# Performance work log

Measured on AMD Instinct MI355X. Metric: run time of the kernel, lower is better.

Reference implementation:

```python
import jax, jax.numpy as jnp
import numpy as np

C = 192          # filter_channels (= in_channels in this module)
K = 3            # kernel_size
NB = 10          # num_bins of rational-quadratic spline (VITS default)
TB = 5.0         # tail_bound
NF = 4           # number of ConvFlow steps per branch
L = 3            # DDSConv n_layers
LOG2PI = float(np.log(2.0 * np.pi))


def conv1x1(x, w, b):
    # x: (B, Cin, T), w: (Cout, Cin)
    return jnp.einsum('oi,bit->bot', w, x) + b[None, :, None]


def depthwise(x, w, b, dil):
    # x: (B, C, T), w: (C, 1, K), dilated depthwise conv, 'same' padding
    pad = dil * (K - 1) // 2
    y = jax.lax.conv_general_dilated(
        x, w, window_strides=(1,), padding=[(pad, pad)], rhs_dilation=(dil,),
        dimension_numbers=('NCH', 'OIH', 'NCH'), feature_group_count=x.shape[1])
    return y + b[None, :, None]


def layer_norm_c(x, g, b, eps=1e-5):
    # VITS LayerNorm: normalize over the channel axis (axis=1)
    m = jnp.mean(x, axis=1, keepdims=True)
    v = jnp.mean((x - m) ** 2, axis=1, keepdims=True)
    return (x - m) * jax.lax.rsqrt(v + eps) * g[None, :, None] + b[None, :, None]


def dds(x, x_mask, g, dep_w, dep_b, pw_w, pw_b, ln_g, ln_b):
    # DDSConv: dilated depth-separable conv stack with residual
    if g is not None:
        x = x + g
    for i in range(L):
        dil = K ** i
        y = depthwise(x * x_mask, dep_w[i], dep_b[i], dil)
        y = jax.nn.gelu(layer_norm_c(y, ln_g[i, 0], ln_b[i, 0]))
        y = conv1x1(y, pw_w[i], pw_b[i])
        y = jax.nn.gelu(layer_norm_c(y, ln_g[i, 1], ln_b[i, 1]))
        x = x + y  # dropout disabled in deterministic reference
    return x * x_mask


def ew_affine(z, x_mask, m, logs):
    y = (m[None, :, None] + jnp.exp(logs)[None, :, None] * z) * x_mask
    ld = jnp.sum(logs[None, :, None] * x_mask, axis=(1, 2))
    return y, ld


def rqs_forward(x_in, uw, uh, ud):
    # unconstrained rational-quadratic spline, forward direction, linear tails
    mb = 1e-3  # min bin width / height / derivative
    const = float(np.log(np.expm1(1.0 - mb)))
    inside = (x_in >= -TB) & (x_in <= TB)
    ud = jnp.pad(ud, ((0, 0), (0, 0), (0, 0), (1, 1)), constant_values=const)
    wd = jax.nn.softmax(uw, -1); wd = mb + (1.0 - mb * NB) * wd
    cw = jnp.cumsum(wd, -1)
    cw = jnp.concatenate([jnp.zeros_like(cw[..., :1]), cw], -1)
    cw = 2.0 * TB * cw - TB
    cw = cw.at[..., 0].set(-TB).at[..., -1].set(TB)
    wd = cw[..., 1:] - cw[..., :-1]
    ht = jax.nn.softmax(uh, -1); ht = mb + (1.0 - mb * NB) * ht
    ch = jnp.cumsum(ht, -1)
    ch = jnp.concatenate([jnp.zeros_like(ch[..., :1]), ch], -1)
    ch = 2.0 * TB * ch - TB
    ch = ch.at[..., 0].set(-TB).at[..., -1].set(TB)
    ht = ch[..., 1:] - ch[..., :-1]
    dv = mb + jax.nn.softplus(ud)  # (..., NB+1)
    xc = jnp.clip(x_in, -TB, TB)
    idx = jnp.clip(jnp.sum((xc[..., None] >= cw[..., :-1]).astype(jnp.int32), -1) - 1, 0, NB - 1)
    g = lambda a, i: jnp.take_along_axis(a, i[..., None], -1)[..., 0]
    icw, iw, ich, ih = g(cw, idx), g(wd, idx), g(ch, idx), g(ht, idx)
    idelta = ih / iw
    d0, d1 = g(dv, idx), g(dv, idx + 1)
    th = (xc - icw) / iw
    t1m = th * (1.0 - th)
    den = idelta + (d0 + d1 - 2.0 * idelta) * t1m
    out = ich + ih * (idelta * th * th + d0 * t1m) / den
    dnum = idelta * idelta * (d1 * th * th + 2.0 * idelta * t1m + d0 * (1.0 - th) ** 2)
    lad = jnp.log(dnum) - 2.0 * jnp.log(den)
    return jnp.where(inside, out, x_in), jnp.where(inside, lad, 0.0)


def conv_flow(z, x_mask, g, pre_w, pre_b, dep_w, dep_b, pw_w, pw_b, ln_g, ln_b, proj_w, proj_b):
    x0, x1 = z[:, :1], z[:, 1:]  # (B,1,T) each
    h = conv1x1(x0, pre_w, pre_b)
    h = dds(h, x_mask, g, dep_w, dep_b, pw_w, pw_b, ln_g, ln_b)
    h = conv1x1(h, proj_w, proj_b) * x_mask      # (B, 3*NB-1, T)
    B, _, T = h.shape
    h = h.reshape(B, 1, 3 * NB - 1, T).transpose(0, 1, 3, 2)  # (B,1,T,3*NB-1)
    s = 1.0 / np.sqrt(C)
    x1n, lad = rqs_forward(x1, h[..., :NB] * s, h[..., NB:2 * NB] * s, h[..., 2 * NB:])
    zo = jnp.concatenate([x0, x1n], 1) * x_mask
    return zo, jnp.sum(lad * x_mask, axis=(1, 2))


def _forward(x, x_mask, w, e_q, pre_w, pre_b, proj_w, proj_b,
             dds_dep_w, dds_dep_b, dds_pw_w, dds_pw_b, dds_ln_g, dds_ln_b,
             post_pre_w, post_pre_b, post_proj_w, post_proj_b,
             pdds_dep_w, pdds_dep_b, pdds_pw_w, pdds_pw_b, pdds_ln_g, pdds_ln_b,
             aff_m, aff_logs,
             f_pre_w, f_pre_b, f_dep_w, f_dep_b, f_pw_w, f_pw_b, f_ln_g, f_ln_b, f_proj_w, f_proj_b,
             paff_m, paff_logs,
             p_pre_w, p_pre_b, p_dep_w, p_dep_b, p_pw_w, p_pw_b, p_ln_g, p_ln_b, p_proj_w, p_proj_b):
    x = jax.lax.stop_gradient(x)
    h = conv1x1(x, pre_w, pre_b)
    h = dds(h, x_mask, None, dds_dep_w, dds_dep_b, dds_pw_w, dds_pw_b, dds_ln_g, dds_ln_b)
    h = conv1x1(h, proj_w, proj_b) * x_mask
    hw = conv1x1(w, post_pre_w, post_pre_b)
    hw = dds(hw, x_mask, None, pdds_dep_w, pdds_dep_b, pdds_pw_w, pdds_pw_b, pdds_ln_g, pdds_ln_b)
    hw = conv1x1(hw, post_proj_w, post_proj_b) * x_mask
    e = e_q * x_mask
    zq, ldq = ew_affine(e, x_mask, paff_m, paff_logs)
    gp = h + hw
    for i in range(NF):
        zq, ld = conv_flow(zq, x_mask, gp, p_pre_w[i], p_pre_b[i], p_dep_w[i], p_dep_b[i],
                           p_pw_w[i], p_pw_b[i], p_ln_g[i], p_ln_b[i], p_proj_w[i], p_proj_b[i])
        ldq = ldq + ld
        zq = zq[:, ::-1]  # Flip (logdet 0)
    zu, z1 = zq[:, :1], zq[:, 1:]
    u = jax.nn.sigmoid(zu) * x_mask
    z0 = (w - u) * x_mask
    ldq = ldq + jnp.sum((jax.nn.log_sigmoid(zu) + jax.nn.log_sigmoid(-zu)) * x_mask, axis=(1, 2))
    logq = jnp.sum(-0.5 * (LOG2PI + e * e) * x_mask, axis=(1, 2)) - ldq
    y0 = jnp.log(jnp.maximum(z0, 1e-5)) * x_mask  # Log flow
    ldt = jnp.sum(-y0, axis=(1, 2))
    z = jnp.concatenate([y0, z1], 1)
    z, ld = ew_affine(z, x_mask, aff_m, aff_logs)
    ldt = ldt + ld
    for i in range(NF):
        z, ld = conv_flow(z, x_mask, h, f_pre_w[i], f_pre_b[i], f_dep_w[i], f_dep_b[i],
                          f_pw_w[i], f_pw_b[i], f_ln_g[i], f_ln_b[i], f_proj_w[i], f_proj_b[i])
        ldt = ldt + ld
        z = z[:, ::-1]
    nll = jnp.sum(0.5 * (LOG2PI + z * z) * x_mask, axis=(1, 2)) - ldt
    return nll + logq  # (B,)


def setup_inputs() -> dict:
    key = jax.random.key(0)
    ks = jax.random.split(key, 24)
    B, T = 32, 768
    P = 3 * NB - 1
    r = lambda k, shape, s=0.05: jax.random.normal(k, shape, jnp.float32) * s
    d = {}
    d['x'] = jax.random.normal(ks[0], (B, C, T), jnp.float32)
    d['x_mask'] = jnp.ones((B, 1, T), jnp.float32)
    d['w'] = jax.random.uniform(ks[1], (B, 1, T), jnp.float32) * 10.0 + 1.0  # positive durations
    d['e_q'] = jax.random.normal(ks[2], (B, 2, T), jnp.float32)
    d['pre_w'] = r(ks[3], (C, C)); d['pre_b'] = jnp.zeros((C,), jnp.float32)
    d['proj_w'] = r(ks[4], (C, C)); d['proj_b'] = jnp.zeros((C,), jnp.float32)
    d['dds_dep_w'] = r(ks[5], (L, C, 1, K)); d['dds_dep_b'] = jnp.zeros((L, C), jnp.float32)
    d['dds_pw_w'] = r(ks[6], (L, C, C)); d['dds_pw_b'] = jnp.zeros((L, C), jnp.float32)
    d['dds_ln_g'] = jnp.ones((L, 2, C), jnp.float32); d['dds_ln_b'] = jnp.zeros((L, 2, C), jnp.float32)
    d['post_pre_w'] = r(ks[7], (C, 1)); d['post_pre_b'] = jnp.zeros((C,), jnp.float32)
    d['post_proj_w'] = r(ks[8], (C, C)); d['post_proj_b'] = jnp.zeros((C,), jnp.float32)
    d['pdds_dep_w'] = r(ks[9], (L, C, 1, K)); d['pdds_dep_b'] = jnp.zeros((L, C), jnp.float32)
    d['pdds_pw_w'] = r(ks[10], (L, C, C)); d['pdds_pw_b'] = jnp.zeros((L, C), jnp.float32)
    d['pdds_ln_g'] = jnp.ones((L, 2, C), jnp.float32); d['pdds_ln_b'] = jnp.zeros((L, 2, C), jnp.float32)
    d['aff_m'] = r(ks[11], (2,)); d['aff_logs'] = r(ks[12], (2,))
    d['f_pre_w'] = r(ks[13], (NF, C, 1)); d['f_pre_b'] = jnp.zeros((NF, C), jnp.float32)
    d['f_dep_w'] = r(ks[14], (NF, L, C, 1, K)); d['f_dep_b'] = jnp.zeros((NF, L, C), jnp.float32)
    d['f_pw_w'] = r(ks[15], (NF, L, C, C)); d['f_pw_b'] = jnp.zeros((NF, L, C), jnp.float32)
    d['f_ln_g'] = jnp.ones((NF, L, 2, C), jnp.float32); d['f_ln_b'] = jnp.zeros((NF, L, 2, C), jnp.float32)
    d['f_proj_w'] = r(ks[16], (NF, P, C), 0.01); d['f_proj_b'] = jnp.zeros((NF, P), jnp.float32)
    d['paff_m'] = r(ks[17], (2,)); d['paff_logs'] = r(ks[18], (2,))
    d['p_pre_w'] = r(ks[19], (NF, C, 1)); d['p_pre_b'] = jnp.zeros((NF, C), jnp.float32)
    d['p_dep_w'] = r(ks[20], (NF, L, C, 1, K)); d['p_dep_b'] = jnp.zeros((NF, L, C), jnp.float32)
    d['p_pw_w'] = r(ks[21], (NF, L, C, C)); d['p_pw_b'] = jnp.zeros((NF, L, C), jnp.float32)
    d['p_ln_g'] = jnp.ones((NF, L, 2, C), jnp.float32); d['p_ln_b'] = jnp.zeros((NF, L, 2, C), jnp.float32)
    d['p_proj_w'] = r(ks[22], (NF, P, C), 0.01); d['p_proj_b'] = jnp.zeros((NF, P), jnp.float32)
    return d


def reference(x, x_mask, w, e_q, pre_w, pre_b, proj_w, proj_b,
              dds_dep_w, dds_dep_b, dds_pw_w, dds_pw_b, dds_ln_g, dds_ln_b,
              post_pre_w, post_pre_b, post_proj_w, post_proj_b,
              pdds_dep_w, pdds_dep_b, pdds_pw_w, pdds_pw_b, pdds_ln_g, pdds_ln_b,
              aff_m, aff_logs,
              f_pre_w, f_pre_b, f_dep_w, f_dep_b, f_pw_w, f_pw_b, f_ln_g, f_ln_b, f_proj_w, f_proj_b,
              paff_m, paff_logs,
              p_pre_w, p_pre_b, p_dep_w, p_dep_b, p_pw_w, p_pw_b, p_ln_g, p_ln_b, p_proj_w, p_proj_b):
    return _forward(x, x_mask, w, e_q, pre_w, pre_b, proj_w, proj_b,
                    dds_dep_w, dds_dep_b, dds_pw_w, dds_pw_b, dds_ln_g, dds_ln_b,
                    post_pre_w, post_pre_b, post_proj_w, post_proj_b,
                    pdds_dep_w, pdds_dep_b, pdds_pw_w, pdds_pw_b, pdds_ln_g, pdds_ln_b,
                    aff_m, aff_logs,
                    f_pre_w, f_pre_b, f_dep_w, f_dep_b, f_pw_w, f_pw_b, f_ln_g, f_ln_b, f_proj_w, f_proj_b,
                    paff_m, paff_logs,
                    p_pre_w, p_pre_b, p_dep_w, p_dep_b, p_pw_w, p_pw_b, p_ln_g, p_ln_b, p_proj_w, p_proj_b)
```

## Files before the change

kernel.cpp:

```cpp
#include <hip/hip_runtime.h>
#include <math.h>

#define CC 192
#define TTT 768
#define PP 29
#define LOG2PI_F 1.8378770664093453f
#define WSLOT 36864
#define PSW 6144
#define XS 200
#define XSP 200
#define PARL 1728

typedef __attribute__((ext_vector_type(8))) short short8;
typedef __attribute__((ext_vector_type(4))) float floatx4;
typedef __attribute__((ext_vector_type(2))) float float2v;
union Frag { int4 i; short8 s; };

__device__ __forceinline__ float2v fma2(float2v a, float2v b, float2v c){
  return __builtin_elementwise_fma(a, b, c);
}
__device__ __forceinline__ float geluf(float x){
  float u = 1.5957691216057308f * (x + 0.044715f*x*x*x);
  return x * __builtin_amdgcn_rcpf(1.f + __expf(-u));
}
__device__ __forceinline__ float softplus_f(float x){
  return (x > 20.f) ? x : log1pf(__expf(x));
// ... 182 lines not shown
  __syncthreads();
  #pragma unroll
  for (int k=0;k<3;k++){
    int task = k*256 + tid;
    int row = task/24, cn = task%24;
    *(int4*)(outb + ((size_t)b*TTT + t0 + row)*CC + cn*8) = *(const int4*)&bufX[row*XS + cn*8];
  }
}

template<int DIL, int SPLITF>
__device__ __forceinline__ void dds_layer(
    unsigned short* __restrict__ ping,
    const float* __restrict__ pl,
    float* __restrict__ pnd, const float* __restrict__ pns,
    const float* __restrict__ mrow,
    float (* __restrict__ sqx)[2][2],
    const unsigned short* __restrict__ WL,
    int tid, int w, int lane, int n16, int quad, int row){
  constexpr int NT = SPLITF ? 6 : 12;
  const int tb = SPLITF ? ((w & 1)*6) : 0;
  const int rowL = SPLITF ? (16 + (w>>1)*16 + n16) : row;
  Frag bfr[6];
  floatx4 acc[NT];
  {
    int iL = rowL - DIL; iL = iL < 0 ? 0 : iL;
    int iR = rowL + DIL; iR = iR > 63 ? 63 : iR;
    float2v vv[24];
    float2v s2v = {0.f,0.f}, q2v = {0.f,0.f};
    #pragma unroll
    for (int j=0;j<6;j++){
      int kk = j*32 + quad*8;
      int4 L4 = *(const int4*)&ping[iL*XSP + kk];
      int4 C4 = *(const int4*)&ping[rowL*XSP + kk];
      int4 R4 = *(const int4*)&ping[iR*XSP + kk];
      unsigned int* Lp = (unsigned int*)&L4;
      unsigned int* Cp = (unsigned int*)&C4;
      unsigned int* Rp = (unsigned int*)&R4;
      float4 w0a = *(const float4*)&pl[kk],       w0b = *(const float4*)&pl[kk+4];
      float4 w1a = *(const float4*)&pl[192+kk],   w1b = *(const float4*)&pl[192+kk+4];
      float4 w2a = *(const float4*)&pl[384+kk],   w2b = *(const float4*)&pl[384+kk+4];
      float4 dba = *(const float4*)&pl[576+kk],   dbb = *(const float4*)&pl[576+kk+4];
// ... 18 lines not shown
      int kk = j*32 + quad*8;
      float4 g0a = *(const float4*)&pl[768+kk], g0b = *(const float4*)&pl[768+kk+4];
      float4 b0a = *(const float4*)&pl[960+kk], b0b = *(const float4*)&pl[960+kk+4];
      unsigned int wwp[4];
      #pragma unroll
      for (int p=0;p<4;p++){
        float2v a = fma2((vv[j*4+p]-mm2)*rr2, pick2(g0a,g0b,p), pick2(b0a,b0b,p));
        wwp[p] = packbf2(geluf(a.x), geluf(a.y));
      }
      bfr[j].i = make_int4((int)wwp[0], (int)wwp[1], (int)wwp[2], (int)wwp[3]);
    }
  }
  __syncthreads();
  if (pns){
    #pragma unroll
    for (int k=0;k<7;k++){
      int i2 = k*256 + tid;
      if (i2 < PARL) pnd[i2] = pns[i2];
    }
  }
  {
    Frag afb[2][6];
    #pragma unroll
    for (int k=0;k<6;k++)
      afb[0][k].i = *(const int4*)(WL + ((size_t)((tb+0)*6 + k)*64 + lane)*8);
    #pragma unroll
    for (int tile=0; tile<NT; tile++){
      int cur = tile & 1, nxt = cur ^ 1;
      if (tile < NT-1){
        #pragma unroll
        for (int k=0;k<6;k++)
          afb[nxt][k].i = *(const int4*)(WL + ((size_t)((tb+tile+1)*6 + k)*64 + lane)*8);
      }
      acc[tile] = (floatx4){0.f,0.f,0.f,0.f};
      #pragma unroll
      for (int k=0;k<6;k++)
        acc[tile] = __builtin_amdgcn_mfma_f32_16x16x32_bf16(afb[cur][k].s, bfr[k].s, acc[tile], 0,0,0);
    }
  }
  float2v s2p = {0.f,0.f}, q2p = {0.f,0.f};
  #pragma unroll
  for (int tile=0; tile<NT; tile++){
    int co = (tb+tile)*16 + quad*4;
    float4 pbv = *(const float4*)&pl[1536+co];
    acc[tile][0] += pbv.x; acc[tile][1] += pbv.y;
    acc[tile][2] += pbv.z; acc[tile][3] += pbv.w;
    float2v v01 = {acc[tile][0], acc[tile][1]};
    float2v v23 = {acc[tile][2], acc[tile][3]};
    s2p += v01 + v23;
    q2p = fma2(v01, v01, q2p);
    q2p = fma2(v23, v23, q2p);
  }
  float s2 = s2p.x + s2p.y, q2 = q2p.x + q2p.y;
  s2 += __shfl_xor(s2, 16); s2 += __shfl_xor(s2, 32);
  q2 += __shfl_xor(q2, 16); q2 += __shfl_xor(q2, 32);
  if constexpr (SPLITF){
    int r16 = rowL - 16;
    if (quad == 0){ sqx[r16][w&1][0] = s2; sqx[r16][w&1][1] = q2; }
    __syncthreads();
    int oh = (w&1)^1;
    s2 += sqx[r16][oh][0];
    q2 += sqx[r16][oh][1];
  }
  float cmP = s2*(1.f/CC);
  float crP = rsqrtf(q2*(1.f/CC) - cmP*cmP + 1e-5f);
  float mc = mrow[rowL];
  float2v mc2 = {mc,mc};
  float2v cm2 = {cmP,cmP}, cr2 = {crP,crP};
  #pragma unroll
  for (int tile=0; tile<NT; tile++){
    int co = (tb+tile)*16 + quad*4;
    float4 g1v = *(const float4*)&pl[1152+co];
    float4 b1v = *(const float4*)&pl[1344+co];
    uint2 ux = *(uint2*)&ping[rowL*XSP + co];
    float2v x01 = unbf2v(ux.x), x23 = unbf2v(ux.y);
    float2v v01 = {acc[tile][0], acc[tile][1]};
    float2v v23 = {acc[tile][2], acc[tile][3]};
    float2v a01 = fma2((v01-cm2)*cr2, (float2v){g1v.x,g1v.y}, (float2v){b1v.x,b1v.y});
    float2v a23 = fma2((v23-cm2)*cr2, (float2v){g1v.z,g1v.w}, (float2v){b1v.z,b1v.w});
    float2v h01 = (x01 + (float2v){geluf(a01.x), geluf(a01.y)}) * mc2;
    float2v h23 = (x23 + (float2v){geluf(a23.x), geluf(a23.y)}) * mc2;
    uint2 wv;
    wv.x = packbf2(h01.x, h01.y);
    wv.y = packbf2(h23.x, h23.y);
    *(uint2*)&ping[rowL*XSP + co] = wv;
  }
  __syncthreads();
}

__global__ __launch_bounds__(256,3) void mega_dds_k(
    const unsigned short* __restrict__ in,
    const float* __restrict__ zsrc, int zstride,
    const unsigned short* __restrict__ g,
    const float* __restrict__ mask,
    const float* __restrict__ parP,
    const float* __restrict__ pw1, const float* __restrict__ pb1,
    const unsigned short* __restrict__ Wsw,
    int srcmode, int outmode,
    const unsigned short* __restrict__ projW, const float* __restrict__ projB,
    float* __restrict__ z, int zs, float* __restrict__ acco,
    const unsigned short* __restrict__ cvW, const float* __restrict__ cvB,
    const unsigned short* __restrict__ addsrc, unsigned short* __restrict__ cvout,
    int cvmode,
    int pmode, int finmode, const float* __restrict__ aux,
    const float* __restrict__ pmv, const float* __restrict__ plv){
  __shared__ unsigned short ping[64*XSP];
  __shared__ float par[2][PARL];
  __shared__ float mrow[64];
  __shared__ float sqx[32][2][2];
  float* pro = par[0];

  int b = blockIdx.y, t0 = blockIdx.x*32, tid = threadIdx.x;
  int ws0 = t0 - 16;
  int w = tid >> 6, lane = tid & 63;
  int n16 = lane & 15, quad = lane >> 4;
  int row = w*16 + n16;
  const float* mkb = mask + (size_t)b*TTT;

  float pm0=0.f, pm1=0.f, lg0=0.f, lg1=0.f, ex0=0.f, ex1=0.f;
  if (pmode){
    pm0 = pmv[0]; pm1 = pmv[1]; lg0 = plv[0]; lg1 = plv[1];
    ex0 = __expf(lg0); ex1 = __expf(lg1);
  }

  if (tid < 64){
    int gt = ws0 + tid;
    bool inr = (gt >= 0) && (gt < TTT);
    int gc = gt < 0 ? 0 : (gt > TTT-1 ? TTT-1 : gt);
    mrow[tid] = inr ? mkb[gc] : 0.f;
  }
  #pragma unroll
  for (int k=0;k<7;k++){
    int i2 = k*256 + tid;
    if (i2 < PARL) par[0][i2] = parP[i2];
  }
  if (srcmode == 0){
    #pragma unroll
    for (int k=0;k<6;k++){
      int task = k*256 + tid;
      int r = task/24, cn = task%24, c0 = cn*8;
      int gt = ws0 + r;
      bool inr = (gt >= 0) && (gt < TTT);
      int gc = gt < 0 ? 0 : (gt > TTT-1 ? TTT-1 : gt);
      float mv = inr ? mkb[gc] : 0.f;
      float hv[8];
      unp8(*(const int4*)(in + ((size_t)b*TTT + gc)*CC + c0), hv);
      int4 pk;
      pk.x = (int)packbf2(hv[0]*mv, hv[1]*mv); pk.y = (int)packbf2(hv[2]*mv, hv[3]*mv);
      pk.z = (int)packbf2(hv[4]*mv, hv[5]*mv); pk.w = (int)packbf2(hv[6]*mv, hv[7]*mv);
      *(int4*)&ping[r*XSP + c0] = pk;
    }
  } else {
    #pragma unroll
    for (int k=0;k<6;k++){
      int task = k*256 + tid;
      int r = task/24, cn = task%24, c0 = cn*8;
      int gt = ws0 + r;
      bool inr = (gt >= 0) && (gt < TTT);
      int gc = gt < 0 ? 0 : (gt > TTT-1 ? TTT-1 : gt);
      float mv = inr ? mkb[gc] : 0.f;
      float zv;
      if (pmode == 1){
        float e0 = aux[((size_t)b*2+0)*TTT + gc] * mv;
        zv = fmaf(ex0, e0, pm0)*mv;
      } else if (pmode == 2){
        float zu = zsrc[(size_t)b*zstride + gc];
        float wv = aux[(size_t)b*TTT + gc];
        float u  = mv / (1.f + __expf(-zu));
        float y0 = logf(fmaxf((wv - u)*mv, 1e-5f))*mv;
        zv = fmaf(ex0, y0, pm0)*mv;
// ... 13 lines not shown
      float4 pbb2 = *(const float4*)(pb1 + c0 + 4);
      float pwv[8], pbv[8];
      f4arr(pwa, pwv); f4arr(pwb2, pwv+4);
      f4arr(pba, pbv); f4arr(pbb2, pbv+4);
      float ov[8];
      #pragma unroll
      for (int e=0;e<8;e++) ov[e] = (hv[e] + fmaf(pwv[e], zv, pbv[e]))*mv;
      int4 pk;
      pk.x = (int)packbf2(ov[0], ov[1]); pk.y = (int)packbf2(ov[2], ov[3]);
      pk.z = (int)packbf2(ov[4], ov[5]); pk.w = (int)packbf2(ov[6], ov[7]);
      *(int4*)&ping[r*XSP + c0] = pk;
    }
  }
  __syncthreads();

  dds_layer<1,0>(ping, par[0], par[1], parP + (size_t)1*PARL, mrow, sqx,
                 Wsw + 0*(size_t)WSLOT, tid, w, lane, n16, quad, row);
  dds_layer<3,0>(ping, par[1], par[0], parP + (size_t)2*PARL, mrow, sqx,
                 Wsw + 1*(size_t)WSLOT, tid, w, lane, n16, quad, row);
  dds_layer<9,1>(ping, par[0], nullptr, nullptr, mrow, sqx,
                 Wsw + 2*(size_t)WSLOT, tid, w, lane, n16, quad, row);

  if (outmode == 2){
    if (cvmode == 2){
      #pragma unroll
      for (int k=0;k<3;k++){
        int task = k*256 + tid;
        int r = task/24, cn = task%24;
        int dr = r + ((r >= 16) ? 32 : 0);
        *(int4*)&ping[dr*XSP + cn*8] =
            *(const int4*)(addsrc + ((size_t)b*TTT + t0 + r)*CC + cn*8);
      }
    }
    Frag af[3][6];
    #pragma unroll
    for (int ct=0; ct<3; ct++){
      int tile = w*3 + ct;
      #pragma unroll
      for (int k=0;k<6;k++)
        af[ct][k].i = *(const int4*)(cvW + ((size_t)(tile*6 + k)*64 + lane)*8);
    }
    floatx4 acc2[3][2];
    #pragma unroll
    for (int ct=0;ct<3;ct++)
      #pragma unroll
      for (int tt=0;tt<2;tt++)
        acc2[ct][tt] = (floatx4){0.f,0.f,0.f,0.f};
    #pragma unroll
    for (int k=0;k<6;k++){
      Frag bf[2];
      #pragma unroll
      for (int tt=0;tt<2;tt++)
        bf[tt].i = *(const int4*)&ping[(16 + tt*16 + n16)*XSP + k*32 + quad*8];
      #pragma unroll
      for (int ct=0;ct<3;ct++)
        #pragma unroll
        for (int tt=0;tt<2;tt++)
          acc2[ct][tt] = __builtin_amdgcn_mfma_f32_16x16x32_bf16(af[ct][k].s, bf[tt].s, acc2[ct][tt], 0,0,0);
    }
    __syncthreads();
    #pragma unroll
    for (int ct=0;ct<3;ct++){
      int cobase = w*48 + ct*16 + quad*4;
      float4 b4 = *(const float4*)(cvB + cobase);
      float ba[4] = {b4.x, b4.y, b4.z, b4.w};
      #pragma unroll
      for (int tt=0;tt<2;tt++){
        int t = tt*16 + n16;
        float mv = mrow[16 + t];
        float av[4] = {0.f,0.f,0.f,0.f};
        if (cvmode == 2){
          int hr = t + ((t >= 16) ? 32 : 0);
          uint2 uy = *(uint2*)&ping[hr*XSP + cobase];
          unbf2(uy.x, av[0], av[1]); unbf2(uy.y, av[2], av[3]);
        }
        float hh[4];
        #pragma unroll
        for (int r=0;r<4;r++){
          float v = (acc2[ct][tt][r] + ba[r]) * mv;
          if (cvmode == 2) v += av[r];
          hh[r] = v;
        }
        uint2 wv; wv.x = packbf2(hh[0], hh[1]); wv.y = packbf2(hh[2], hh[3]);
        *(uint2*)&ping[(16 + t)*XSP + cobase] = wv;
      }
    }
    __syncthreads();
    #pragma unroll
    for (int k=0;k<3;k++){
      int task = k*256 + tid;
      int r = task/24, cn = task%24, c0 = cn*8;
      *(int4*)(cvout + ((size_t)b*TTT + t0 + r)*CC + c0) = *(const int4*)&ping[(16+r)*XSP + c0];
    }
    return;
  }

  {
    int ctp = w & 1;
    int prow = 16 + (w>>1)*16 + n16;
    Frag afp[6];
    #pragma unroll
    for (int k=0;k<6;k++)
      afp[k].i = *(const int4*)(projW + ((size_t)(ctp*6 + k)*64 + lane)*8);
    Frag bfp[6];
    #pragma unroll
    for (int k=0;k<6;k++)
      bfp[k].i = *(const int4*)&ping[prow*XSP + k*32 + quad*8];
    floatx4 acc2 = (floatx4){0.f,0.f,0.f,0.f};
    #pragma unroll
    for (int k=0;k<6;k++)
      acc2 = __builtin_amdgcn_mfma_f32_16x16x32_bf16(afp[k].s, bfp[k].s, acc2, 0,0,0);
    int rt = prow - 16;
    float mv = mrow[prow];
    #pragma unroll
    for (int r=0;r<4;r++){
      int co = ctp*16 + quad*4 + r;
      if (co < PP) pro[rt*30 + co] = (acc2[r] + projB[co]) * mv;
    }
  }
  __syncthreads();
  if (tid < 32){
    const float scv = 0.07216878364870323f;
    int tg = t0 + tid;
    float m = mrow[16+tid];
    float* z0p = z + ((size_t)b*2 + zs)*TTT + tg;
    float* z1p = z + ((size_t)b*2 + (1-zs))*TTT + tg;
    float xs, zwr0, extra = 0.f;
    if (pmode == 1){
      float e0c = aux[((size_t)b*2+0)*TTT + tg]*m;
      float e1c = aux[((size_t)b*2+1)*TTT + tg]*m;
      zwr0 = fmaf(ex0, e0c, pm0)*m;
      xs   = fmaf(ex1, e1c, pm1)*m;
      extra = -0.5f*(LOG2PI_F + e0c*e0c)*m - 0.5f*(LOG2PI_F + e1c*e1c)*m - (lg0+lg1)*m;
    } else if (pmode == 2){
      xs = fmaf(ex1, *z1p, pm1)*m;
      zwr0 = (*z0p)*m;
    } else if (pmode == 3){
      float zu = *z1p;
      float wv = aux[(size_t)b*TTT + tg];
      float u  = m/(1.f + __expf(-zu));
      float y0 = logf(fmaxf((wv - u)*m, 1e-5f))*m;
      xs = fmaf(ex0, y0, pm0)*m;
      extra = -(logsig_f(zu)+logsig_f(-zu))*m + y0 - (lg0+lg1)*m;
      zwr0 = (*z0p)*m;
    } else {
      xs = *z1p;
      zwr0 = (*z0p)*m;
    }
    float uw[10], uh[10], ud[9];
    #pragma unroll
    for (int k=0;k<10;k++) uw[k]=pro[tid*30+k]*scv;
    #pragma unroll
    for (int k=0;k<10;k++) uh[k]=pro[tid*30+10+k]*scv;
    #pragma unroll
    for (int k=0;k<9;k++)  ud[k]=pro[tid*30+20+k];
    bool inside = (xs >= -5.f) && (xs <= 5.f);
    float xc = fminf(fmaxf(xs,-5.f),5.f);
    float mx=uw[0];
    #pragma unroll
    for (int k=1;k<10;k++) mx=fmaxf(mx,uw[k]);
    float sw=0.f; float wd[10];
    #pragma unroll
    for (int k=0;k<10;k++){ wd[k]=__expf(uw[k]-mx); sw+=wd[k]; }
    float invw = 1.f/sw;
    #pragma unroll
    for (int k=0;k<10;k++) wd[k]=fmaf(0.99f*invw, wd[k], 1e-3f);
    float mh=uh[0];
    #pragma unroll
    for (int k=1;k<10;k++) mh=fmaxf(mh,uh[k]);
    float sh=0.f; float ht[10];
    #pragma unroll
    for (int k=0;k<10;k++){ ht[k]=__expf(uh[k]-mh); sh+=ht[k]; }
    float invh = 1.f/sh;
    #pragma unroll
    for (int k=0;k<10;k++) ht[k]=fmaf(0.99f*invh, ht[k], 1e-3f);
    float cw=-5.f, icw=-5.f, iw=1.f; int idx=0;
    #pragma unroll
    for (int i2=0;i2<10;i2++){
      float nw = (i2==9) ? 5.f : fmaf(10.f, wd[i2], cw);
      if (cw <= xc){ idx=i2; icw=cw; iw=nw-cw; }
      cw=nw;
    }
    float ch=-5.f, ich=-5.f, ih=1.f;
    #pragma unroll
    for (int i2=0;i2<10;i2++){
      float nh = (i2==9) ? 5.f : fmaf(10.f, ht[i2], ch);
      if (i2==idx){ ich=ch; ih=nh-ch; }
      ch=nh;
    }
    const float UDC = logf(expm1f(0.999f));
    float d0=1.f, d1=1.f;
    #pragma unroll
    for (int k=0;k<11;k++){
      float uu = (k==0 || k==10) ? UDC : ud[k-1];
      float dk = 1e-3f + softplus_f(uu);
      if (k==idx)   d0=dk;
      if (k==idx+1) d1=dk;
    }
    float idel = ih/iw;
    float th = (xc-icw)/iw;
    float t1m = th*(1.f-th);
    float den = idel + (d0+d1-2.f*idel)*t1m;
    float outv = ich + ih*(idel*th*th + d0*t1m)/den;
    float omt = 1.f-th;
    float dnum = idel*idel*(d1*th*th + 2.f*idel*t1m + d0*omt*omt);
    float lad = logf(dnum) - 2.f*logf(den);
    float y = inside ? outv : xs;
    lad = inside ? lad : 0.f;
    float y1 = y*m;
    *z1p = y1;
    *z0p = zwr0;
    if (finmode){
      extra += 0.5f*(LOG2PI_F + y1*y1)*m + 0.5f*(LOG2PI_F + zwr0*zwr0)*m;
    }
    float c = extra - lad*m;
    c += __shfl_xor(c, 1); c += __shfl_xor(c, 2);
    c += __shfl_xor(c, 4); c += __shfl_xor(c, 8);
    c += __shfl_xor(c, 16);
    if (tid == 0) atomicAdd(acco + b, c);
  }
}

__global__ void write_out_k(const float* __restrict__ acc, float* __restrict__ out, int n){
  int i = threadIdx.x;
  if (i < n) out[i] = acc[i];
}

extern "C" void kernel_launch(void* const* d_in, const int* in_sizes, int n_in,
                              void* d_out, int out_size, void* d_ws, size_t ws_size,
                              hipStream_t stream){
  (void)n_in; (void)out_size; (void)ws_size;
  const float* x         = (const float*)d_in[0];
  const float* mask      = (const float*)d_in[1];
// ... 55 lines not shown
  size_t wtot = 33*(size_t)WSLOT + 8*(size_t)PSW;
  float* parP = (float*)(Wb + ((wtot + 7) & ~(size_t)7));
  float* zbuf = parP + 30*(size_t)PARL;
  float* acc  = zbuf + (size_t)Bn*2*TTT;

  hipMemsetAsync(acc, 0, Bn*sizeof(float), stream);
  convert_w_k<<<(int)((wtot + 255)/256), 256, 0, stream>>>(
      pre_w, proj_w, post_proj_w, dds_pw_w, pdds_pw_w, p_pw_w, f_pw_w,
      p_proj_w, f_proj_w, Wb);
  pack_par_k<<<(30*PARL + 255)/256, 256, 0, stream>>>(
      dds_dep_w, dds_dep_b, dds_ln_g, dds_ln_b, dds_pw_b,
      pdds_dep_w, pdds_dep_b, pdds_ln_g, pdds_ln_b, pdds_pw_b,
      p_dep_w, p_dep_b, p_ln_g, p_ln_b, p_pw_b,
      f_dep_w, f_dep_b, f_ln_g, f_ln_b, f_pw_b, parP);

  dim3 g32(TTT/32, Bn);
  dim3 b256(256);

  unsigned short* W_pre      = Wb + 0*(size_t)WSLOT;
  unsigned short* W_proj     = Wb + 1*(size_t)WSLOT;
  unsigned short* W_postproj = Wb + 2*(size_t)WSLOT;
  unsigned short* W_dds      = Wb + 3*(size_t)WSLOT;
  unsigned short* W_pdds     = Wb + 6*(size_t)WSLOT;
  unsigned short* W_ppw      = Wb + 9*(size_t)WSLOT;
  unsigned short* W_fpw      = Wb + 21*(size_t)WSLOT;
  unsigned short* W_pproj    = Wb + 33*(size_t)WSLOT;
  unsigned short* W_fproj    = W_pproj + 4*(size_t)PSW;

  trans_conv_k<<<g32, b256, 0, stream>>>(x, W_pre, pre_b, A);
  mega_dds_k<<<g32, b256, 0, stream>>>(A, nullptr, 0, nullptr, mask,
      parP + 0*(size_t)3*PARL, nullptr, nullptr,
      W_dds, 0, 2, nullptr, nullptr, nullptr, 0, acc,
      W_proj, proj_b, nullptr, H, 1,
      0, 0, nullptr, nullptr, nullptr);

  mega_dds_k<<<g32, b256, 0, stream>>>(nullptr, w_in, TTT, nullptr, mask,
      parP + 1*(size_t)3*PARL, post_pre_w, post_pre_b,
      W_pdds, 1, 2, nullptr, nullptr, nullptr, 0, acc,
      W_postproj, post_proj_b, H, GP, 2,
      0, 0, nullptr, nullptr, nullptr);

  for (int f=0; f<4; f++){
    int s = f & 1;
    mega_dds_k<<<g32, b256, 0, stream>>>(nullptr, zbuf + (size_t)s*TTT, 2*TTT, GP, mask,
        parP + (size_t)(2+f)*3*PARL,
        p_pre_w + (size_t)f*CC, p_pre_b + (size_t)f*CC,
        W_ppw + (size_t)f*3*WSLOT, 1, 1,
        W_pproj + (size_t)f*PSW, p_proj_b + (size_t)f*PP, zbuf, s, acc,
        nullptr, nullptr, nullptr, nullptr, 0,
        (f==0) ? 1 : 0, 0, e_q, paff_m, paff_logs);
  }

  for (int f=0; f<4; f++){
    int s = f & 1;
    int pmode = (f==0) ? 2 : ((f==1) ? 3 : 0);
    mega_dds_k<<<g32, b256, 0, stream>>>(nullptr, zbuf + (size_t)s*TTT, 2*TTT, H, mask,
        parP + (size_t)(6+f)*3*PARL,
        f_pre_w + (size_t)f*CC, f_pre_b + (size_t)f*CC,
        W_fpw + (size_t)f*3*WSLOT, 1, 1,
        W_fproj + (size_t)f*PSW, f_proj_b + (size_t)f*PP, zbuf, s, acc,
        nullptr, nullptr, nullptr, nullptr, 0,
        pmode, (f==3) ? 1 : 0, w_in, aff_m, aff_logs);
  }

  write_out_k<<<1, 64, 0, stream>>>(acc, (float*)d_out, Bn);
}
```

Measured before the change: 676.3 us.

## Widen DDS tile to 48 output timesteps with 320-thread blocks

Each block of the fused DDS kernel now produces 48 timesteps instead of 32, using an 80-row window (16-step halo on each side) and 5 wavefronts. This shrinks the share of halo rows that are recomputed at every layer. The last dilated layer no longer splits channels across wave pairs with a shared-memory reduction; three waves each handle 16 full rows and the rest stay idle. The output conv and projection stages are reorganised the same way. The cost is idle waves in later stages and fewer blocks in the grid, which lowers occupancy.

```diff
diff --git a/kernel.cpp b/kernel.cpp
--- a/kernel.cpp
+++ b/kernel.cpp
@@ -10,6 +10,9 @@
 #define XS 200
 #define XSP 200
 #define PARL 1728
+#define NTH 320
+#define WIN 80
+#define OUT 48
 
 typedef __attribute__((ext_vector_type(8))) short short8;
 typedef __attribute__((ext_vector_type(4))) float floatx4;
@@ -222,17 +225,15 @@
     const float* __restrict__ pl,
     float* __restrict__ pnd, const float* __restrict__ pns,
     const float* __restrict__ mrow,
-    float (* __restrict__ sqx)[2][2],
     const unsigned short* __restrict__ WL,
     int tid, int w, int lane, int n16, int quad, int row){
-  constexpr int NT = SPLITF ? 6 : 12;
-  const int tb = SPLITF ? ((w & 1)*6) : 0;
-  const int rowL = SPLITF ? (16 + (w>>1)*16 + n16) : row;
+  const bool active = (!SPLITF) || (w < 3);
+  const int rowL = SPLITF ? (16 + (w < 3 ? w : 0)*16 + n16) : row;
   Frag bfr[6];
-  floatx4 acc[NT];
-  {
+  floatx4 acc[12];
+  if (active){
     int iL = rowL - DIL; iL = iL < 0 ? 0 : iL;
-    int iR = rowL + DIL; iR = iR > 63 ? 63 : iR;
+    int iR = rowL + DIL; iR = iR > WIN-1 ? WIN-1 : iR;
     float2v vv[24];
     float2v s2v = {0.f,0.f}, q2v = {0.f,0.f};
     #pragma unroll
@@ -281,81 +282,75 @@
   __syncthreads();
   if (pns){
     #pragma unroll
-    for (int k=0;k<7;k++){
-      int i2 = k*256 + tid;
+    for (int k=0;k<6;k++){
+      int i2 = k*NTH + tid;
       if (i2 < PARL) pnd[i2] = pns[i2];
     }
   }
-  {
-    Frag afb[2][6];
-    #pragma unroll
-    for (int k=0;k<6;k++)
-      afb[0][k].i = *(const int4*)(WL + ((size_t)((tb+0)*6 + k)*64 + lane)*8);
-    #pragma unroll
-    for (int tile=0; tile<NT; tile++){
-      int cur = tile & 1, nxt = cur ^ 1;
-      if (tile < NT-1){
+  if (active){
+    {
+      Frag afb[2][6];
+      #pragma unroll
+      for (int k=0;k<6;k++)
+        afb[0][k].i = *(const int4*)(WL + ((size_t)(0*6 + k)*64 + lane)*8);
+      #pragma unroll
+      for (int tile=0; tile<12; tile++){
+        int cur = tile & 1, nxt = cur ^ 1;
+        if (tile < 11){
+          #pragma unroll
+          for (int k=0;k<6;k++)
+            afb[nxt][k].i = *(const int4*)(WL + ((size_t)((tile+1)*6 + k)*64 + lane)*8);
+        }
+        acc[tile] = (floatx4){0.f,0.f,0.f,0.f};
         #pragma unroll
         for (int k=0;k<6;k++)
-          afb[nxt][k].i = *(const int4*)(WL + ((size_t)((tb+tile+1)*6 + k)*64 + lane)*8);
-      }
-      acc[tile] = (floatx4){0.f,0.f,0.f,0.f};
-      #pragma unroll
-      for (int k=0;k<6;k++)
-        acc[tile] = __builtin_amdgcn_mfma_f32_16x16x32_bf16(afb[cur][k].s, bfr[k].s, acc[tile], 0,0,0);
-    }
-  }
-  float2v s2p = {0.f,0.f}, q2p = {0.f,0.f};
-  #pragma unroll
-  for (int tile=0; tile<NT; tile++){
-    int co = (tb+tile)*16 + quad*4;
-    float4 pbv = *(const float4*)&pl[1536+co];
-    acc[tile][0] += pbv.x; acc[tile][1] += pbv.y;
-    acc[tile][2] += pbv.z; acc[tile][3] += pbv.w;
-    float2v v01 = {acc[tile][0], acc[tile][1]};
-    float2v v23 = {acc[tile][2], acc[tile][3]};
-    s2p += v01 + v23;
-    q2p = fma2(v01, v01, q2p);
-    q2p = fma2(v23, v23, q2p);
-  }
-  float s2 = s2p.x + s2p.y, q2 = q2p.x + q2p.y;
-  s2 += __shfl_xor(s2, 16); s2 += __shfl_xor(s2, 32);
-  q2 += __shfl_xor(q2, 16); q2 += __shfl_xor(q2, 32);
-  if constexpr (SPLITF){
-    int r16 = rowL - 16;
-    if (quad == 0){ sqx[r16][w&1][0] = s2; sqx[r16][w&1][1] = q2; }
-    __syncthreads();
-    int oh = (w&1)^1;
-    s2 += sqx[r16][oh][0];
-    q2 += sqx[r16][oh][1];
-  }
-  float cmP = s2*(1.f/CC);
-  float crP = rsqrtf(q2*(1.f/CC) - cmP*cmP + 1e-5f);
-  float mc = mrow[rowL];
-  float2v mc2 = {mc,mc};
-  float2v cm2 = {cmP,cmP}, cr2 = {crP,crP};
-  #pragma unroll
-  for (int tile=0; tile<NT; tile++){
-    int co = (tb+tile)*16 + quad*4;
-    float4 g1v = *(const float4*)&pl[1152+co];
-    float4 b1v = *(const float4*)&pl[1344+co];
-    uint2 ux = *(uint2*)&ping[rowL*XSP + co];
-    float2v x01 = unbf2v(ux.x), x23 = unbf2v(ux.y);
-    float2v v01 = {acc[tile][0], acc[tile][1]};
-    float2v v23 = {acc[tile][2], acc[tile][3]};
-    float2v a01 = fma2((v01-cm2)*cr2, (float2v){g1v.x,g1v.y}, (float2v){b1v.x,b1v.y});
-    float2v a23 = fma2((v23-cm2)*cr2, (float2v){g1v.z,g1v.w}, (float2v){b1v.z,b1v.w});
-    float2v h01 = (x01 + (float2v){geluf(a01.x), geluf(a01.y)}) * mc2;
-    float2v h23 = (x23 + (float2v){geluf(a23.x), geluf(a23.y)}) * mc2;
-    uint2 wv;
-    wv.x = packbf2(h01.x, h01.y);
-    wv.y = packbf2(h23.x, h23.y);
-    *(uint2*)&ping[rowL*XSP + co] = wv;
+          acc[tile] = __builtin_amdgcn_mfma_f32_16x16x32_bf16(afb[cur][k].s, bfr[k].s, acc[tile], 0,0,0);
+      }
+    }
+    float2v s2p = {0.f,0.f}, q2p = {0.f,0.f};
+    #pragma unroll
+    for (int tile=0; tile<12; tile++){
+      int co = tile*16 + quad*4;
+      float4 pbv = *(const float4*)&pl[1536+co];
+      acc[tile][0] += pbv.x; acc[tile][1] += pbv.y;
+      acc[tile][2] += pbv.z; acc[tile][3] += pbv.w;
+      float2v v01 = {acc[tile][0], acc[tile][1]};
+      float2v v23 = {acc[tile][2], acc[tile][3]};
+      s2p += v01 + v23;
+      q2p = fma2(v01, v01, q2p);
+      q2p = fma2(v23, v23, q2p);
+    }
+    float s2 = s2p.x + s2p.y, q2 = q2p.x + q2p.y;
+    s2 += __shfl_xor(s2, 16); s2 += __shfl_xor(s2, 32);
+    q2 += __shfl_xor(q2, 16); q2 += __shfl_xor(q2, 32);
+    float cmP = s2*(1.f/CC);
+    float crP = rsqrtf(q2*(1.f/CC) - cmP*cmP + 1e-5f);
+    float mc = mrow[rowL];
+    float2v mc2 = {mc,mc};
+    float2v cm2 = {cmP,cmP}, cr2 = {crP,crP};
+    #pragma unroll
+    for (int tile=0; tile<12; tile++){
+      int co = tile*16 + quad*4;
+      float4 g1v = *(const float4*)&pl[1152+co];
+      float4 b1v = *(const float4*)&pl[1344+co];
+      uint2 ux = *(uint2*)&ping[rowL*XSP + co];
+      float2v x01 = unbf2v(ux.x), x23 = unbf2v(ux.y);
+      float2v v01 = {acc[tile][0], acc[tile][1]};
+      float2v v23 = {acc[tile][2], acc[tile][3]};
+      float2v a01 = fma2((v01-cm2)*cr2, (float2v){g1v.x,g1v.y}, (float2v){b1v.x,b1v.y});
+      float2v a23 = fma2((v23-cm2)*cr2, (float2v){g1v.z,g1v.w}, (float2v){b1v.z,b1v.w});
+      float2v h01 = (x01 + (float2v){geluf(a01.x), geluf(a01.y)}) * mc2;
+      float2v h23 = (x23 + (float2v){geluf(a23.x), geluf(a23.y)}) * mc2;
+      uint2 wv;
+      wv.x = packbf2(h01.x, h01.y);
+      wv.y = packbf2(h23.x, h23.y);
+      *(uint2*)&ping[rowL*XSP + co] = wv;
+    }
   }
   __syncthreads();
 }
 
-__global__ __launch_bounds__(256,3) void mega_dds_k(
+__global__ __launch_bounds__(NTH,3) void mega_dds_k(
     const unsigned short* __restrict__ in,
     const float* __restrict__ zsrc, int zstride,
     const unsigned short* __restrict__ g,
@@ -371,13 +366,12 @@
     int cvmode,
     int pmode, int finmode, const float* __restrict__ aux,
     const float* __restrict__ pmv, const float* __restrict__ plv){
-  __shared__ unsigned short ping[64*XSP];
+  __shared__ unsigned short ping[WIN*XSP];
   __shared__ float par[2][PARL];
-  __shared__ float mrow[64];
-  __shared__ float sqx[32][2][2];
+  __shared__ float mrow[WIN];
   float* pro = par[0];
 
-  int b = blockIdx.y, t0 = blockIdx.x*32, tid = threadIdx.x;
+  int b = blockIdx.y, t0 = blockIdx.x*OUT, tid = threadIdx.x;
   int ws0 = t0 - 16;
   int w = tid >> 6, lane = tid & 63;
   int n16 = lane & 15, quad = lane >> 4;
@@ -390,21 +384,21 @@
     ex0 = __expf(lg0); ex1 = __expf(lg1);
   }
 
-  if (tid < 64){
+  if (tid < WIN){
     int gt = ws0 + tid;
     bool inr = (gt >= 0) && (gt < TTT);
     int gc = gt < 0 ? 0 : (gt > TTT-1 ? TTT-1 : gt);
     mrow[tid] = inr ? mkb[gc] : 0.f;
   }
   #pragma unroll
-  for (int k=0;k<7;k++){
-    int i2 = k*256 + tid;
+  for (int k=0;k<6;k++){
+    int i2 = k*NTH + tid;
     if (i2 < PARL) par[0][i2] = parP[i2];
   }
   if (srcmode == 0){
     #pragma unroll
     for (int k=0;k<6;k++){
-      int task = k*256 + tid;
+      int task = k*NTH + tid;
       int r = task/24, cn = task%24, c0 = cn*8;
       int gt = ws0 + r;
       bool inr = (gt >= 0) && (gt < TTT);
@@ -420,7 +414,7 @@
   } else {
     #pragma unroll
     for (int k=0;k<6;k++){
-      int task = k*256 + tid;
+      int task = k*NTH + tid;
       int r = task/24, cn = task%24, c0 = cn*8;
       int gt = ws0 + r;
       bool inr = (gt >= 0) && (gt < TTT);
@@ -464,209 +458,209 @@
   }
   __syncthreads();
 
-  dds_layer<1,0>(ping, par[0], par[1], parP + (size_t)1*PARL, mrow, sqx,
+  dds_layer<1,0>(ping, par[0], par[1], parP + (size_t)1*PARL, mrow,
                  Wsw + 0*(size_t)WSLOT, tid, w, lane, n16, quad, row);
-  dds_layer<3,0>(ping, par[1], par[0], parP + (size_t)2*PARL, mrow, sqx,
+  dds_layer<3,0>(ping, par[1], par[0], parP + (size_t)2*PARL, mrow,
                  Wsw + 1*(size_t)WSLOT, tid, w, lane, n16, quad, row);
-  dds_layer<9,1>(ping, par[0], nullptr, nullptr, mrow, sqx,
+  dds_layer<9,1>(ping, par[0], nullptr, nullptr, mrow,
                  Wsw + 2*(size_t)WSLOT, tid, w, lane, n16, quad, row);
 
   if (outmode == 2){
-    if (cvmode == 2){
-      #pragma unroll
-      for (int k=0;k<3;k++){
-        int task = k*256 + tid;
-        int r = task/24, cn = task%24;
-        int dr = r + ((r >= 16) ? 32 : 0);
-        *(int4*)&ping[dr*XSP + cn*8] =
-            *(const int4*)(addsrc + ((size_t)b*TTT + t0 + r)*CC + cn*8);
-      }
-    }
-    Frag af[3][6];
-    #pragma unroll
-    for (int ct=0; ct<3; ct++){
-      int tile = w*3 + ct;
-      #pragma unroll
-      for (int k=0;k<6;k++)
-        af[ct][k].i = *(const int4*)(cvW + ((size_t)(tile*6 + k)*64 + lane)*8);
-    }
-    floatx4 acc2[3][2];
-    #pragma unroll
-    for (int ct=0;ct<3;ct++)
-      #pragma unroll
-      for (int tt=0;tt<2;tt++)
-        acc2[ct][tt] = (floatx4){0.f,0.f,0.f,0.f};
-    #pragma unroll
-    for (int k=0;k<6;k++){
-      Frag bf[2];
-      #pragma unroll
-      for (int tt=0;tt<2;tt++)
-        bf[tt].i = *(const int4*)&ping[(16 + tt*16 + n16)*XSP + k*32 + quad*8];
+    if (w < 4){
+      Frag af[3][6];
+      #pragma unroll
+      for (int ct=0; ct<3; ct++){
+        int tile = w*3 + ct;
+        #pragma unroll
+        for (int k=0;k<6;k++)
+          af[ct][k].i = *(const int4*)(cvW + ((size_t)(tile*6 + k)*64 + lane)*8);
+      }
+      floatx4 acc2[3][3];
       #pragma unroll
       for (int ct=0;ct<3;ct++)
         #pragma unroll
-        for (int tt=0;tt<2;tt++)
-          acc2[ct][tt] = __builtin_amdgcn_mfma_f32_16x16x32_bf16(af[ct][k].s, bf[tt].s, acc2[ct][tt], 0,0,0);
+        for (int tt=0;tt<3;tt++)
+          acc2[ct][tt] = (floatx4){0.f,0.f,0.f,0.f};
+      #pragma unroll
+      for (int k=0;k<6;k++){
+        Frag bf[3];
+        #pragma unroll
+        for (int tt=0;tt<3;tt++)
+          bf[tt].i = *(const int4*)&ping[(16 + tt*16 + n16)*XSP + k*32 + quad*8];
+        #pragma unroll
+        for (int ct=0;ct<3;ct++)
+          #pragma unroll
+          for (int tt=0;tt<3;tt++)
+            acc2[ct][tt] = __builtin_amdgcn_mfma_f32_16x16x32_bf16(af[ct][k].s, bf[tt].s, acc2[ct][tt], 0,0,0);
+      }
+      __syncthreads();
+      #pragma unroll
+      for (int ct=0;ct<3;ct++){
+        int cobase = w*48 + ct*16 + quad*4;
+        float4 b4 = *(const float4*)(cvB + cobase);
+        float ba[4] = {b4.x, b4.y, b4.z, b4.w};
+        #pragma unroll
+        for (int tt=0;tt<3;tt++){
+          int t = tt*16 + n16;
+          float mv = mrow[16 + t];
+          float av[4] = {0.f,0.f,0.f,0.f};
+          if (cvmode == 2){
+            uint2 uy = *(const uint2*)(addsrc + ((size_t)b*TTT + t0 + t)*CC + cobase);
+            unbf2(uy.x, av[0], av[1]); unbf2(uy.y, av[2], av[3]);
+          }
+          float hh[4];
+          #pragma unroll
+          for (int r=0;r<4;r++){
+            float v = (acc2[ct][tt][r] + ba[r]) * mv;
+            if (cvmode == 2) v += av[r];
+            hh[r] = v;
+          }
+          uint2 wv; wv.x = packbf2(hh[0], hh[1]); wv.y = packbf2(hh[2], hh[3]);
+          *(uint2*)&ping[(16 + t)*XSP + cobase] = wv;
+        }
+      }
+    } else {
+      __syncthreads();
     }
     __syncthreads();
     #pragma unroll
-    for (int ct=0;ct<3;ct++){
-      int cobase = w*48 + ct*16 + quad*4;
-      float4 b4 = *(const float4*)(cvB + cobase);
-      float ba[4] = {b4.x, b4.y, b4.z, b4.w};
-      #pragma unroll
-      for (int tt=0;tt<2;tt++){
-        int t = tt*16 + n16;
-        float mv = mrow[16 + t];
-        float av[4] = {0.f,0.f,0.f,0.f};
-        if (cvmode == 2){
-          int hr = t + ((t >= 16) ? 32 : 0);
-          uint2 uy = *(uint2*)&ping[hr*XSP + cobase];
-          unbf2(uy.x, av[0], av[1]); unbf2(uy.y, av[2], av[3]);
-        }
-        float hh[4];
-        #pragma unroll
-        for (int r=0;r<4;r++){
-          float v = (acc2[ct][tt][r] + ba[r]) * mv;
-          if (cvmode == 2) v += av[r];
-          hh[r] = v;
-        }
-        uint2 wv; wv.x = packbf2(hh[0], hh[1]); wv.y = packbf2(hh[2], hh[3]);
-        *(uint2*)&ping[(16 + t)*XSP + cobase] = wv;
-      }
-    }
-    __syncthreads();
-    #pragma unroll
-    for (int k=0;k<3;k++){
-      int task = k*256 + tid;
-      int r = task/24, cn = task%24, c0 = cn*8;
-      *(int4*)(cvout + ((size_t)b*TTT + t0 + r)*CC + c0) = *(const int4*)&ping[(16+r)*XSP + c0];
+    for (int k=0;k<4;k++){
+      int task = k*NTH + tid;
+      if (task < OUT*24){
+        int r = task/24, cn = task%24, c0 = cn*8;
+        *(int4*)(cvout + ((size_t)b*TTT + t0 + r)*CC + c0) = *(const int4*)&ping[(16+r)*XSP + c0];
+      }
     }
     return;
   }
 
-  {
-    int ctp = w & 1;
-    int prow = 16 + (w>>1)*16 + n16;
-    Frag afp[6];
-    #pragma unroll
-    for (int k=0;k<6;k++)
-      afp[k].i = *(const int4*)(projW + ((size_t)(ctp*6 + k)*64 + lane)*8);
+  if (w < 3){
+    int prow = 16 + w*16 + n16;
     Frag bfp[6];
     #pragma unroll
     for (int k=0;k<6;k++)
       bfp[k].i = *(const int4*)&ping[prow*XSP + k*32 + quad*8];
-    floatx4 acc2 = (floatx4){0.f,0.f,0.f,0.f};
-    #pragma unroll
-    for (int k=0;k<6;k++)
-      acc2 = __builtin_amdgcn_mfma_f32_16x16x32_bf16(afp[k].s, bfp[k].s, acc2, 0,0,0);
     int rt = prow - 16;
     float mv = mrow[prow];
     #pragma unroll
-    for (int r=0;r<4;r++){
-      int co = ctp*16 + quad*4 + r;
-      if (co < PP) pro[rt*30 + co] = (acc2[r] + projB[co]) * mv;
+    for (int ctp=0; ctp<2; ctp++){
+      floatx4 acc2 = (floatx4){0.f,0.f,0.f,0.f};
+      #pragma unroll
+      for (int k=0;k<6;k++){
+        Frag afp;
+        afp.i = *(const int4*)(projW + ((size_t)(ctp*6 + k)*64 + lane)*8);
+        acc2 = __builtin_amdgcn_mfma_f32_16x16x32_bf16(afp.s, bfp[k].s, acc2, 0,0,0);
+      }
+      #pragma unroll
+      for (int r=0;r<4;r++){
+        int co = ctp*16 + quad*4 + r;
+        if (co < PP) pro[rt*30 + co] = (acc2[r] + projB[co]) * mv;
+      }
     }
   }
   __syncthreads();
-  if (tid < 32){
-    const float scv = 0.07216878364870323f;
-    int tg = t0 + tid;
-    float m = mrow[16+tid];
-    float* z0p = z + ((size_t)b*2 + zs)*TTT + tg;
-    float* z1p = z + ((size_t)b*2 + (1-zs))*TTT + tg;
-    float xs, zwr0, extra = 0.f;
-    if (pmode == 1){
-      float e0c = aux[((size_t)b*2+0)*TTT + tg]*m;
-      float e1c = aux[((size_t)b*2+1)*TTT + tg]*m;
-      zwr0 = fmaf(ex0, e0c, pm0)*m;
-      xs   = fmaf(ex1, e1c, pm1)*m;
-      extra = -0.5f*(LOG2PI_F + e0c*e0c)*m - 0.5f*(LOG2PI_F + e1c*e1c)*m - (lg0+lg1)*m;
-    } else if (pmode == 2){
-      xs = fmaf(ex1, *z1p, pm1)*m;
-      zwr0 = (*z0p)*m;
-    } else if (pmode == 3){
-      float zu = *z1p;
-      float wv = aux[(size_t)b*TTT + tg];
-      float u  = m/(1.f + __expf(-zu));
-      float y0 = logf(fmaxf((wv - u)*m, 1e-5f))*m;
-      xs = fmaf(ex0, y0, pm0)*m;
-      extra = -(logsig_f(zu)+logsig_f(-zu))*m + y0 - (lg0+lg1)*m;
-      zwr0 = (*z0p)*m;
-    } else {
-      xs = *z1p;
-      zwr0 = (*z0p)*m;
-    }
-    float uw[10], uh[10], ud[9];
-    #pragma unroll
-    for (int k=0;k<10;k++) uw[k]=pro[tid*30+k]*scv;
-    #pragma unroll
-    for (int k=0;k<10;k++) uh[k]=pro[tid*30+10+k]*scv;
-    #pragma unroll
-    for (int k=0;k<9;k++)  ud[k]=pro[tid*30+20+k];
-    bool inside = (xs >= -5.f) && (xs <= 5.f);
-    float xc = fminf(fmaxf(xs,-5.f),5.f);
-    float mx=uw[0];
-    #pragma unroll
-    for (int k=1;k<10;k++) mx=fmaxf(mx,uw[k]);
-    float sw=0.f; float wd[10];
-    #pragma unroll
-    for (int k=0;k<10;k++){ wd[k]=__expf(uw[k]-mx); sw+=wd[k]; }
-    float invw = 1.f/sw;
-    #pragma unroll
-    for (int k=0;k<10;k++) wd[k]=fmaf(0.99f*invw, wd[k], 1e-3f);
-    float mh=uh[0];
-    #pragma unroll
-    for (int k=1;k<10;k++) mh=fmaxf(mh,uh[k]);
-    float sh=0.f; float ht[10];
-    #pragma unroll
-    for (int k=0;k<10;k++){ ht[k]=__expf(uh[k]-mh); sh+=ht[k]; }
-    float invh = 1.f/sh;
-    #pragma unroll
-    for (int k=0;k<10;k++) ht[k]=fmaf(0.99f*invh, ht[k], 1e-3f);
-    float cw=-5.f, icw=-5.f, iw=1.f; int idx=0;
-    #pragma unroll
-    for (int i2=0;i2<10;i2++){
-      float nw = (i2==9) ? 5.f : fmaf(10.f, wd[i2], cw);
-      if (cw <= xc){ idx=i2; icw=cw; iw=nw-cw; }
-      cw=nw;
-    }
-    float ch=-5.f, ich=-5.f, ih=1.f;
-    #pragma unroll
-    for (int i2=0;i2<10;i2++){
-      float nh = (i2==9) ? 5.f : fmaf(10.f, ht[i2], ch);
-      if (i2==idx){ ich=ch; ih=nh-ch; }
-      ch=nh;
-    }
-    const float UDC = logf(expm1f(0.999f));
-    float d0=1.f, d1=1.f;
-    #pragma unroll
-    for (int k=0;k<11;k++){
-      float uu = (k==0 || k==10) ? UDC : ud[k-1];
-      float dk = 1e-3f + softplus_f(uu);
-      if (k==idx)   d0=dk;
-      if (k==idx+1) d1=dk;
-    }
-    float idel = ih/iw;
-    float th = (xc-icw)/iw;
-    float t1m = th*(1.f-th);
-    float den = idel + (d0+d1-2.f*idel)*t1m;
-    float outv = ich + ih*(idel*th*th + d0*t1m)/den;
-    float omt = 1.f-th;
-    float dnum = idel*idel*(d1*th*th + 2.f*idel*t1m + d0*omt*omt);
-    float lad = logf(dnum) - 2.f*logf(den);
-    float y = inside ? outv : xs;
-    lad = inside ? lad : 0.f;
-    float y1 = y*m;
-    *z1p = y1;
-    *z0p = zwr0;
-    if (finmode){
-      extra += 0.5f*(LOG2PI_F + y1*y1)*m + 0.5f*(LOG2PI_F + zwr0*zwr0)*m;
-    }
-    float c = extra - lad*m;
+  if (tid < 64){
+    float c = 0.f;
+    if (tid < OUT){
+      const float scv = 0.07216878364870323f;
+      int t = tid;
+      int tg = t0 + t;
+      float m = mrow[16+t];
+      float* z0p = z + ((size_t)b*2 + zs)*TTT + tg;
+      float* z1p = z + ((size_t)b*2 + (1-zs))*TTT + tg;
+      float xs, zwr0, extra = 0.f;
+      if (pmode == 1){
+        float e0c = aux[((size_t)b*2+0)*TTT + tg]*m;
+        float e1c = aux[((size_t)b*2+1)*TTT + tg]*m;
+        zwr0 = fmaf(ex0, e0c, pm0)*m;
+        xs   = fmaf(ex1, e1c, pm1)*m;
+        extra = -0.5f*(LOG2PI_F + e0c*e0c)*m - 0.5f*(LOG2PI_F + e1c*e1c)*m - (lg0+lg1)*m;
+      } else if (pmode == 2){
+        xs = fmaf(ex1, *z1p, pm1)*m;
+        zwr0 = (*z0p)*m;
+      } else if (pmode == 3){
+        float zu = *z1p;
+        float wv = aux[(size_t)b*TTT + tg];
+        float u  = m/(1.f + __expf(-zu));
+        float y0 = logf(fmaxf((wv - u)*m, 1e-5f))*m;
+        xs = fmaf(ex0, y0, pm0)*m;
+        extra = -(logsig_f(zu)+logsig_f(-zu))*m + y0 - (lg0+lg1)*m;
+        zwr0 = (*z0p)*m;
+      } else {
+        xs = *z1p;
+        zwr0 = (*z0p)*m;
+      }
+      float uw[10], uh[10], ud[9];
+      #pragma unroll
+      for (int k=0;k<10;k++) uw[k]=pro[t*30+k]*scv;
+      #pragma unroll
+      for (int k=0;k<10;k++) uh[k]=pro[t*30+10+k]*scv;
+      #pragma unroll
+      for (int k=0;k<9;k++)  ud[k]=pro[t*30+20+k];
+      bool inside = (xs >= -5.f) && (xs <= 5.f);
+      float xc = fminf(fmaxf(xs,-5.f),5.f);
+      float mx=uw[0];
+      #pragma unroll
+      for (int k=1;k<10;k++) mx=fmaxf(mx,uw[k]);
+      float sw=0.f; float wd[10];
+      #pragma unroll
+      for (int k=0;k<10;k++){ wd[k]=__expf(uw[k]-mx); sw+=wd[k]; }
+      float invw = 1.f/sw;
+      #pragma unroll
+      for (int k=0;k<10;k++) wd[k]=fmaf(0.99f*invw, wd[k], 1e-3f);
+      float mh=uh[0];
+      #pragma unroll
+      for (int k=1;k<10;k++) mh=fmaxf(mh,uh[k]);
+      float sh=0.f; float ht[10];
+      #pragma unroll
+      for (int k=0;k<10;k++){ ht[k]=__expf(uh[k]-mh); sh+=ht[k]; }
+      float invh = 1.f/sh;
+      #pragma unroll
+      for (int k=0;k<10;k++) ht[k]=fmaf(0.99f*invh, ht[k], 1e-3f);
+      float cw=-5.f, icw=-5.f, iw=1.f; int idx=0;
+      #pragma unroll
+      for (int i2=0;i2<10;i2++){
+        float nw = (i2==9) ? 5.f : fmaf(10.f, wd[i2], cw);
+        if (cw <= xc){ idx=i2; icw=cw; iw=nw-cw; }
+        cw=nw;
+      }
+      float ch=-5.f, ich=-5.f, ih=1.f;
+      #pragma unroll
+      for (int i2=0;i2<10;i2++){
+        float nh = (i2==9) ? 5.f : fmaf(10.f, ht[i2], ch);
+        if (i2==idx){ ich=ch; ih=nh-ch; }
+        ch=nh;
+      }
+      const float UDC = logf(expm1f(0.999f));
+      float d0=1.f, d1=1.f;
+      #pragma unroll
+      for (int k=0;k<11;k++){
+        float uu = (k==0 || k==10) ? UDC : ud[k-1];
+        float dk = 1e-3f + softplus_f(uu);
+        if (k==idx)   d0=dk;
+        if (k==idx+1) d1=dk;
+      }
+      float idel = ih/iw;
+      float th = (xc-icw)/iw;
+      float t1m = th*(1.f-th);
+      float den = idel + (d0+d1-2.f*idel)*t1m;
+      float outv = ich + ih*(idel*th*th + d0*t1m)/den;
+      float omt = 1.f-th;
+      float dnum = idel*idel*(d1*th*th + 2.f*idel*t1m + d0*omt*omt);
+      float lad = logf(dnum) - 2.f*logf(den);
+      float y = inside ? outv : xs;
+      lad = inside ? lad : 0.f;
+      float y1 = y*m;
+      *z1p = y1;
+      *z0p = zwr0;
+      if (finmode){
+        extra += 0.5f*(LOG2PI_F + y1*y1)*m + 0.5f*(LOG2PI_F + zwr0*zwr0)*m;
+      }
+      c = extra - lad*m;
+    }
     c += __shfl_xor(c, 1); c += __shfl_xor(c, 2);
     c += __shfl_xor(c, 4); c += __shfl_xor(c, 8);
-    c += __shfl_xor(c, 16);
+    c += __shfl_xor(c, 16); c += __shfl_xor(c, 32);
     if (tid == 0) atomicAdd(acco + b, c);
   }
 }
@@ -752,8 +746,8 @@
       p_dep_w, p_dep_b, p_ln_g, p_ln_b, p_pw_b,
       f_dep_w, f_dep_b, f_ln_g, f_ln_b, f_pw_b, parP);
 
-  dim3 g32(TTT/32, Bn);
-  dim3 b256(256);
+  dim3 g32(TTT/32, Bn), g48(TTT/OUT, Bn);
+  dim3 b256(256), b320(NTH);
 
   unsigned short* W_pre      = Wb + 0*(size_t)WSLOT;
   unsigned short* W_proj     = Wb + 1*(size_t)WSLOT;
@@ -766,13 +760,13 @@
   unsigned short* W_fproj    = W_pproj + 4*(size_t)PSW;
 
   trans_conv_k<<<g32, b256, 0, stream>>>(x, W_pre, pre_b, A);
-  mega_dds_k<<<g32, b256, 0, stream>>>(A, nullptr, 0, nullptr, mask,
+  mega_dds_k<<<g48, b320, 0, stream>>>(A, nullptr, 0, nullptr, mask,
       parP + 0*(size_t)3*PARL, nullptr, nullptr,
       W_dds, 0, 2, nullptr, nullptr, nullptr, 0, acc,
       W_proj, proj_b, nullptr, H, 1,
       0, 0, nullptr, nullptr, nullptr);
 
-  mega_dds_k<<<g32, b256, 0, stream>>>(nullptr, w_in, TTT, nullptr, mask,
+  mega_dds_k<<<g48, b320, 0, stream>>>(nullptr, w_in, TTT, nullptr, mask,
       parP + 1*(size_t)3*PARL, post_pre_w, post_pre_b,
       W_pdds, 1, 2, nullptr, nullptr, nullptr, 0, acc,
       W_postproj, post_proj_b, H, GP, 2,
@@ -780,7 +774,7 @@
 
   for (int f=0; f<4; f++){
     int s = f & 1;
-    mega_dds_k<<<g32, b256, 0, stream>>>(nullptr, zbuf + (size_t)s*TTT, 2*TTT, GP, mask,
+    mega_dds_k<<<g48, b320, 0, stream>>>(nullptr, zbuf + (size_t)s*TTT, 2*TTT, GP, mask,
         parP + (size_t)(2+f)*3*PARL,
         p_pre_w + (size_t)f*CC, p_pre_b + (size_t)f*CC,
         W_ppw + (size_t)f*3*WSLOT, 1, 1,
@@ -792,7 +786,7 @@
   for (int f=0; f<4; f++){
     int s = f & 1;
     int pmode = (f==0) ? 2 : ((f==1) ? 3 : 0);
-    mega_dds_k<<<g32, b256, 0, stream>>>(nullptr, zbuf + (size_t)s*TTT, 2*TTT, H, mask,
+    mega_dds_k<<<g48, b320, 0, stream>>>(nullptr, zbuf + (size_t)s*TTT, 2*TTT, H, mask,
         parP + (size_t)(6+f)*3*PARL,
         f_pre_w + (size_t)f*CC, f_pre_b + (size_t)f*CC,
         W_fpw + (size_t)f*3*WSLOT, 1, 1,
```

Measured after the change: 870.4 us. 28.7% more time.
